# Kernel optimization log

Measured on AMD Instinct MI355X. Metric: run time of the kernel, lower is better.

Reference implementation:

```python
import jax, jax.numpy as jnp
import numpy as np

D = 2048
H = 16
HD = D // H
EPS = 1e-5

def setup_inputs() -> dict:
    key = jax.random.key(0)
    ks = jax.random.split(key, 7)
    B, S = 4, 2048
    scale = 1.0 / np.sqrt(D)
    return {
        "hidden_states": jax.random.normal(ks[0], (B, S, D), dtype=jnp.float32),
        "ln_gamma": jnp.ones((D,), dtype=jnp.float32),
        "ln_beta": jnp.zeros((D,), dtype=jnp.float32),
        "W_qkv": jax.random.normal(ks[1], (D, 3 * D), dtype=jnp.float32) * scale,
        "b_qkv": jnp.zeros((3 * D,), dtype=jnp.float32),
        "W_proj": jax.random.normal(ks[2], (D, D), dtype=jnp.float32) * scale,
        "b_proj": jnp.zeros((D,), dtype=jnp.float32),
    }

def reference(hidden_states, ln_gamma, ln_beta, W_qkv, b_qkv, W_proj, b_proj):
    B, S, _ = hidden_states.shape
    # LayerNorm (fused into QKV projection in the original kernel)
    mu = jnp.mean(hidden_states, axis=-1, keepdims=True)
    var = jnp.mean(jnp.square(hidden_states - mu), axis=-1, keepdims=True)
    x = (hidden_states - mu) * jax.lax.rsqrt(var + EPS) * ln_gamma + ln_beta
    # QKV projection
    qkv = jnp.einsum("bsd,de->bse", x, W_qkv) + b_qkv  # [B,S,3D]
    q, k, v = jnp.split(qkv, 3, axis=-1)
    # split heads -> [B,H,S,hd]
    q = q.reshape(B, S, H, HD).transpose(0, 2, 1, 3)
    k = k.reshape(B, S, H, HD).transpose(0, 2, 1, 3)
    v = v.reshape(B, S, H, HD).transpose(0, 2, 1, 3)
    # scaled causal attention
    scores = jnp.einsum("bhqd,bhkd->bhqk", q, k) / jnp.asarray(np.sqrt(HD), q.dtype)
    causal = jnp.tril(jnp.ones((S, S), dtype=bool))
    neg = jnp.finfo(scores.dtype).min
    scores = jnp.where(causal, scores, neg)
    attn = jax.nn.softmax(scores, axis=-1)
    out = jnp.einsum("bhqk,bhkd->bhqd", attn, v)
    # merge heads, output projection (dropout is identity in eval / p=0)
    out = out.transpose(0, 2, 1, 3).reshape(B, S, D)
    return jnp.einsum("bsd,de->bse", out, W_proj) + b_proj
```

## Files before the change

### kernel.cpp

```cpp
#include <hip/hip_runtime.h>
#include <cstdint>

typedef __attribute__((ext_vector_type(8))) short bf16x8;
typedef __attribute__((ext_vector_type(4))) float f32x4;
typedef unsigned short u16;
typedef unsigned int u32;

constexpr int D   = 2048;
constexpr int H   = 16;
constexpr int HD  = 128;
constexpr int BATCH = 4;
constexpr int S   = 2048;
constexpr int ROWS = BATCH * S;
constexpr int N3D = 3 * D;
constexpr int QKW = 2 * D;

__device__ __forceinline__ u16 f2bf(float f) {
    union { float f; u32 u; } v; v.f = f;
    u32 r = v.u + 0x7FFFu + ((v.u >> 16) & 1u);
    return (u16)(r >> 16);
}

__device__ __forceinline__ void gld_lds16(const u16* g, u16* l) {
    __builtin_amdgcn_global_load_lds(
        (const __attribute__((address_space(1))) void*)g,
        (__attribute__((address_space(3))) void*)l, 16, 0, 0);
}

__global__ __launch_bounds__(256) void ln_bf16_kernel(
    const float* __restrict__ x, const float* __restrict__ gamma,
    const float* __restrict__ beta, u16* __restrict__ out)
{
    const int row = blockIdx.x;
    const int t = threadIdx.x;
    const float* xr = x + (size_t)row * D;
    float4 a = ((const float4*)xr)[2*t];
    float4 b = ((const float4*)xr)[2*t+1];
    float s  = a.x+a.y+a.z+a.w + b.x+b.y+b.z+b.w;
    float ss = a.x*a.x+a.y*a.y+a.z*a.z+a.w*a.w + b.x*b.x+b.y*b.y+b.z*b.z+b.w*b.w;
    #pragma unroll
    for (int off = 32; off > 0; off >>= 1) {
        s  += __shfl_down(s, off);
        ss += __shfl_down(ss, off);
    }
    __shared__ float red[8];
    const int wave = t >> 6, lane = t & 63;
    if (lane == 0) { red[wave] = s; red[4+wave] = ss; }
    __syncthreads();
    const float mu   = (red[0]+red[1]+red[2]+red[3]) * (1.0f/D);
    const float var  = (red[4]+red[5]+red[6]+red[7]) * (1.0f/D) - mu*mu;
    const float rstd = rsqrtf(var + 1e-5f);
    float4 g0  = ((const float4*)gamma)[2*t];
    float4 g1  = ((const float4*)gamma)[2*t+1];
    float4 be0 = ((const float4*)beta)[2*t];
    float4 be1 = ((const float4*)beta)[2*t+1];
    union { uint4 v; u16 e[8]; } o;
    o.e[0] = f2bf((a.x-mu)*rstd*g0.x + be0.x);
    o.e[1] = f2bf((a.y-mu)*rstd*g0.y + be0.y);
    o.e[2] = f2bf((a.z-mu)*rstd*g0.z + be0.z);
    o.e[3] = f2bf((a.w-mu)*rstd*g0.w + be0.w);
    o.e[4] = f2bf((b.x-mu)*rstd*g1.x + be1.x);
    o.e[5] = f2bf((b.y-mu)*rstd*g1.y + be1.y);
    o.e[6] = f2bf((b.z-mu)*rstd*g1.z + be1.z);
    o.e[7] = f2bf((b.w-mu)*rstd*g1.w + be1.w);
    ((uint4*)(out + (size_t)row*D))[t] = o.v;
}

__global__ __launch_bounds__(256) void transpose_bf16_kernel(
    const float* __restrict__ in, u16* __restrict__ out, int K, int N)
{
    __shared__ u16 tile[64][65];
    const int tn0 = blockIdx.x * 64;
    const int tk0 = blockIdx.y * 64;
    const int t = threadIdx.x;
    const int tx = t & 63;
    const int ty = t >> 6;
    #pragma unroll
    for (int i = 0; i < 16; i++) {
        int k = ty + i*4;
        tile[k][tx] = f2bf(in[(size_t)(tk0+k)*N + tn0 + tx]);
    }
    __syncthreads();
    #pragma unroll
    for (int i = 0; i < 16; i++) {
        int n = ty + i*4;
        out[(size_t)(tn0+n)*K + tk0 + tx] = tile[tx][n];
    }
}

constexpr int BM = 256, BN = 256, BK = 32;

template<int MODE>
__global__ __launch_bounds__(512, 2) void gemm256_kernel(
    const u16* __restrict__ A, const u16* __restrict__ Bt,
    const float* __restrict__ bias, void* __restrict__ Cout,
    u16* __restrict__ vtb, int M, int N, int K)
{
    __shared__ u16 sA[4 * 8192];
    __shared__ u16 sB[4 * 8192];

    const int t = threadIdx.x;
    const int wave = t >> 6, lane = t & 63;
    const int lr = lane & 15, lq = lane >> 4;
    const int wm = wave >> 2, wn = wave & 3;
    const int m0 = blockIdx.y * BM, n0 = blockIdx.x * BN;

    const int g0 = t, g1 = t + 512;
    const int cs0 = ((g0 & 3) ^ ((g0 >> 3) & 3)) * 8;
    const int cs1 = ((g1 & 3) ^ ((g1 >> 3) & 3)) * 8;
    const u16* gA0 = A  + (size_t)(m0 + (g0 >> 2)) * K + cs0;
    const u16* gA1 = A  + (size_t)(m0 + (g1 >> 2)) * K + cs1;
    const u16* gB0 = Bt + (size_t)(n0 + (g0 >> 2)) * K + cs0;
    const u16* gB1 = Bt + (size_t)(n0 + (g1 >> 2)) * K + cs1;

    f32x4 acc[8][4];
    #pragma unroll
    for (int i = 0; i < 8; i++)
        #pragma unroll
        for (int j = 0; j < 4; j++)
            acc[i][j] = (f32x4)(0.0f);

    const int NT = K / BK;

    auto STAGE_A = [&](int slot, int kt) {
        u16* a = sA + slot * 8192 + wave * 512;
        gld_lds16(gA0 + kt * BK, a);
        gld_lds16(gA1 + kt * BK, a + 4096);
    };
    auto STAGE_B = [&](int slot, int kt) {
        u16* b = sB + slot * 8192 + wave * 512;
        gld_lds16(gB0 + kt * BK, b);
        gld_lds16(gB1 + kt * BK, b + 4096);
    };

    STAGE_A(0, 0); STAGE_B(0, 0);
    STAGE_A(1, 1); STAGE_B(1, 1);
    STAGE_A(2, 2); STAGE_B(2, 2);
    asm volatile("s_waitcnt vmcnt(8)" ::: "memory");
    __builtin_amdgcn_s_barrier();

    const int rblk = (lq ^ ((lr >> 1) & 3)) * 8;

    for (int kt = 0; kt < NT; ++kt) {
        const int tp = (kt + 3 < NT) ? (kt + 3) : (NT - 1);
        const int slot3 = (kt + 3) & 3;
        const u16* tAp = sA + (kt & 3) * 8192 + (wm * 128) * BK + rblk;
        const u16* tBp = sB + (kt & 3) * 8192 + (wn * 64)  * BK + rblk;

        bf16x8 bfr[4], af[4];
        #pragma unroll
        for (int nt = 0; nt < 4; nt++)
            bfr[nt] = *(const bf16x8*)(tBp + (nt * 16 + lr) * BK);
        #pragma unroll
        for (int mt = 0; mt < 4; mt++)
            af[mt] = *(const bf16x8*)(tAp + (mt * 16 + lr) * BK);
        STAGE_A(slot3, tp);
        __builtin_amdgcn_sched_barrier(0);
        __builtin_amdgcn_s_barrier();
        asm volatile("s_waitcnt lgkmcnt(0)" ::: "memory");
        __builtin_amdgcn_sched_barrier(0);
        __builtin_amdgcn_s_setprio(1);
        #pragma unroll
        for (int mt = 0; mt < 4; mt++)
            #pragma unroll
            for (int nt = 0; nt < 4; nt++)
                acc[mt][nt] = __builtin_amdgcn_mfma_f32_16x16x32_bf16(
                    af[mt], bfr[nt], acc[mt][nt], 0, 0, 0);
        __builtin_amdgcn_s_setprio(0);
        __builtin_amdgcn_sched_barrier(0);
        __builtin_amdgcn_s_barrier();

        #pragma unroll
        for (int mt = 0; mt < 4; mt++)
            af[mt] = *(const bf16x8*)(tAp + (64 + mt * 16 + lr) * BK);
        STAGE_B(slot3, tp);
        asm volatile("s_waitcnt vmcnt(8)" ::: "memory");
        __builtin_amdgcn_sched_barrier(0);
        __builtin_amdgcn_s_barrier();
        asm volatile("s_waitcnt lgkmcnt(0)" ::: "memory");
        __builtin_amdgcn_sched_barrier(0);
        __builtin_amdgcn_s_setprio(1);
        #pragma unroll
        for (int mt = 0; mt < 4; mt++)
            #pragma unroll
            for (int nt = 0; nt < 4; nt++)
                acc[4 + mt][nt] = __builtin_amdgcn_mfma_f32_16x16x32_bf16(
                    af[mt], bfr[nt], acc[4 + mt][nt], 0, 0, 0);
        __builtin_amdgcn_s_setprio(0);
        __builtin_amdgcn_sched_barrier(0);
        __builtin_amdgcn_s_barrier();
    }
    asm volatile("s_waitcnt vmcnt(0)" ::: "memory");

    #pragma unroll
    for (int i = 0; i < 8; i++) {
        const int row0 = m0 + wm * 128 + (i >> 2) * 64 + (i & 3) * 16 + lq * 4;
        #pragma unroll
        for (int nt = 0; nt < 4; nt++) {
            const int col = n0 + wn * 64 + nt * 16 + lr;
            const float bv = bias[col];
            float v[4];
            #pragma unroll
            for (int r = 0; r < 4; r++) v[r] = acc[i][nt][r] + bv;
            if (MODE == 0) {
                #pragma unroll
                for (int r = 0; r < 4; r++)
                    ((float*)Cout)[(size_t)(row0 + r) * N + col] = v[r];
            } else {
                if (n0 < QKW) {
                    #pragma unroll
                    for (int r = 0; r < 4; r++)
                        ((u16*)Cout)[(size_t)(row0 + r) * QKW + col] = f2bf(v[r]);
                } else {
                    const int vcol = col - QKW;
                    const int b = row0 >> 11, s0 = row0 & 2047;
                    ushort4 pk;
                    pk.x = f2bf(v[0]); pk.y = f2bf(v[1]);
                    pk.z = f2bf(v[2]); pk.w = f2bf(v[3]);
                    *(ushort4*)(vtb + ((size_t)(b*H + (vcol >> 7)) * HD
                                       + (vcol & 127)) * S + s0) = pk;
                }
            }
        }
    }
}

constexpr int TQ = 64, TK = 64;
constexpr int KPAD = 136;
constexpr int VPAD = 72;
constexpr int PPAD = 72;

__global__ __launch_bounds__(256) void attn_kernel(
    const u16* __restrict__ qkb, const u16* __restrict__ vtb,
    u16* __restrict__ ctx)
{
    __shared__ u16 sK[TK * KPAD];
    __shared__ u16 sVT[HD * VPAD];
    __shared__ u16 sP[4 * 16 * PPAD];

    const int flat = blockIdx.x;
    const int qt = 31 - (flat >> 6);
    const int bh = flat & 63;
    const int b  = bh >> 4, h = bh & 15;
    const int q0 = qt * TQ;
    const int t = threadIdx.x;
    const int wave = t >> 6, lane = t & 63;
    const int lr = lane & 15, lq = lane >> 4;

    const u16* baseQK = qkb + (size_t)b * S * QKW + h * HD;
    const u16* baseVT = vtb + (size_t)bh * HD * S;

    const int qrow = q0 + wave * 16 + lr;
    bf16x8 qf[4];
    #pragma unroll
    for (int kc = 0; kc < 4; kc++)
        qf[kc] = *(const bf16x8*)(baseQK + (size_t)qrow * QKW + kc*32 + lq*8);

    float m_r[4], l_r[4];
    f32x4 o[8];
    #pragma unroll
    for (int r = 0; r < 4; r++) { m_r[r] = -1e30f; l_r[r] = 0.0f; }
    #pragma unroll
    for (int j = 0; j < 8; j++) o[j] = (f32x4)(0.0f);

    const float scale = 0.08838834764831845f;
    const int nkt = qt + 1;

    for (int kt = 0; kt < nkt; kt++) {
        __syncthreads();
        #pragma unroll
        for (int i = 0; i < 4; i++) {
            int c = t + i * 256;
            int krow = c >> 4, kcol = (c & 15) * 8;
            uint4 v = *(const uint4*)(baseQK + D + (size_t)(kt*TK + krow) * QKW + kcol);
            *(uint4*)(sK + krow * KPAD + kcol) = v;
        }
        #pragma unroll
        for (int i = 0; i < 4; i++) {
            int c = t + i * 256;
            int vrow = c >> 3, coff = (c & 7) * 8;
            uint4 v = *(const uint4*)(baseVT + (size_t)vrow * S + kt*TK + coff);
            *(uint4*)(sVT + vrow * VPAD + coff) = v;
        }
        __syncthreads();

        f32x4 sc[4];
        #pragma unroll
        for (int nt = 0; nt < 4; nt++) sc[nt] = (f32x4)(0.0f);
        #pragma unroll
        for (int nt = 0; nt < 4; nt++)
            #pragma unroll
            for (int kc = 0; kc < 4; kc++) {
                bf16x8 kf = *(const bf16x8*)(sK + (nt*16 + lr) * KPAD + kc*32 + lq*8);
                sc[nt] = __builtin_amdgcn_mfma_f32_16x16x32_bf16(qf[kc], kf, sc[nt], 0, 0, 0);
            }

        const bool diag = (kt == qt);
        float rowmax[4] = {-1e30f, -1e30f, -1e30f, -1e30f};
        const int qgb = q0 + wave*16 + lq*4;
        #pragma unroll
        for (int nt = 0; nt < 4; nt++)
            #pragma unroll
            for (int r = 0; r < 4; r++) {
                float sv = sc[nt][r] * scale;
                if (diag) {
                    const int kg = kt*TK + nt*16 + lr;
                    if (kg > qgb + r) sv = -1e30f;
                }
                sc[nt][r] = sv;
                rowmax[r] = fmaxf(rowmax[r], sv);
            }
        #pragma unroll
        for (int mask = 1; mask < 16; mask <<= 1)
            #pragma unroll
            for (int r = 0; r < 4; r++)
                rowmax[r] = fmaxf(rowmax[r], __shfl_xor(rowmax[r], mask));

        float alpha[4];
        #pragma unroll
        for (int r = 0; r < 4; r++) {
            float nm = fmaxf(m_r[r], rowmax[r]);
            alpha[r] = __expf(m_r[r] - nm);
            m_r[r] = nm;
        }

        u16* pw = sP + wave * 16 * PPAD;
        #pragma unroll
        for (int nt = 0; nt < 4; nt++) {
            #pragma unroll
            for (int r = 0; r < 4; r++) {
                float p = __expf(sc[nt][r] - m_r[r]);
                sc[nt][r] = p;
                pw[(lq*4 + r) * PPAD + nt*16 + lr] = f2bf(p);
            }
        }
        #pragma unroll
        for (int r = 0; r < 4; r++) {
            float psum = sc[0][r] + sc[1][r] + sc[2][r] + sc[3][r];
            l_r[r] = l_r[r] * alpha[r] + psum;
        }
        #pragma unroll
        for (int j = 0; j < 8; j++)
            #pragma unroll
            for (int r = 0; r < 4; r++)
                o[j][r] *= alpha[r];

        #pragma unroll
        for (int kc2 = 0; kc2 < 2; kc2++) {
            bf16x8 pa = *(const bf16x8*)(pw + lr * PPAD + kc2*32 + lq*8);
            #pragma unroll
            for (int n2 = 0; n2 < 8; n2++) {
                bf16x8 vb = *(const bf16x8*)(sVT + (n2*16 + lr) * VPAD + kc2*32 + lq*8);
                o[n2] = __builtin_amdgcn_mfma_f32_16x16x32_bf16(pa, vb, o[n2], 0, 0, 0);
            }
        }
    }

    #pragma unroll
    for (int mask = 1; mask < 16; mask <<= 1)
        #pragma unroll
        for (int r = 0; r < 4; r++)
            l_r[r] += __shfl_xor(l_r[r], mask);
    float inv_l[4];
    #pragma unroll
    for (int r = 0; r < 4; r++) inv_l[r] = 1.0f / l_r[r];
    #pragma unroll
    for (int n2 = 0; n2 < 8; n2++)
        #pragma unroll
        for (int r = 0; r < 4; r++) {
            const int qg = q0 + wave*16 + lq*4 + r;
            const float v = o[n2][r] * inv_l[r];
            ctx[(size_t)(b * S + qg) * D + h * HD + n2*16 + lr] = f2bf(v);
        }
}

extern "C" void kernel_launch(void* const* d_in, const int* in_sizes, int n_in,
                              void* d_out, int out_size, void* d_ws, size_t ws_size,
                              hipStream_t stream) {
    const float* hs    = (const float*)d_in[0];
    const float* gamma = (const float*)d_in[1];
    const float* beta  = (const float*)d_in[2];
    const float* Wqkv  = (const float*)d_in[3];
    const float* bqkv  = (const float*)d_in[4];
    const float* Wproj = (const float*)d_in[5];
    const float* bproj = (const float*)d_in[6];

    char* ws = (char*)d_ws;
    size_t off = 0;
    u16* xb   = (u16*)(ws + off); off += (size_t)ROWS * D * 2;
    u16* wtq  = (u16*)(ws + off); off += (size_t)N3D * D * 2;
    u16* wtp  = (u16*)(ws + off); off += (size_t)D * D * 2;
    u16* qkb  = (u16*)(ws + off); off += (size_t)ROWS * QKW * 2;
    u16* vtb  = (u16*)(ws + off); off += (size_t)ROWS * D * 2;
    u16* ctxb = (u16*)(ws + off);

    ln_bf16_kernel<<<ROWS, 256, 0, stream>>>(hs, gamma, beta, xb);
    transpose_bf16_kernel<<<dim3(N3D/64, D/64), 256, 0, stream>>>(Wqkv, wtq, D, N3D);
    transpose_bf16_kernel<<<dim3(D/64,   D/64), 256, 0, stream>>>(Wproj, wtp, D, D);
    gemm256_kernel<2><<<dim3(N3D/BN, ROWS/BM), 512, 0, stream>>>(
        xb, wtq, bqkv, qkb, vtb, ROWS, N3D, D);
    attn_kernel<<<dim3((S/TQ) * BATCH * H), 256, 0, stream>>>(qkb, vtb, ctxb);
    gemm256_kernel<0><<<dim3(D/BN, ROWS/BM), 512, 0, stream>>>(
        ctxb, wtp, bproj, (float*)d_out, nullptr, ROWS, D, D);
}
```

Measured before the change: 610.3 us.

## Double-buffer attention K/V tiles with async LDS loads and swizzled layout

The attention kernel now stages K and V^T tiles directly into LDS with global_load_lds, using two buffers so the next tile is fetched while the current one is computed. This removes the register round-trip and one barrier per iteration. The padded LDS rows are replaced by XOR-swizzled unpadded rows to avoid bank conflicts, and s_setprio raises wave priority around the MFMA loops. The change relies on the async loads being complete before the single remaining barrier, and it doubles LDS use for K and V, which may lower occupancy.

```diff
diff --git a/kernel.cpp b/kernel.cpp
--- a/kernel.cpp
+++ b/kernel.cpp
@@ -226,16 +226,14 @@
 }
 
 constexpr int TQ = 64, TK = 64;
-constexpr int KPAD = 136;
-constexpr int VPAD = 72;
 constexpr int PPAD = 72;
 
 __global__ __launch_bounds__(256) void attn_kernel(
     const u16* __restrict__ qkb, const u16* __restrict__ vtb,
     u16* __restrict__ ctx)
 {
-    __shared__ u16 sK[TK * KPAD];
-    __shared__ u16 sVT[HD * VPAD];
+    __shared__ u16 sK[2 * TK * HD];
+    __shared__ u16 sVT[2 * HD * TK];
     __shared__ u16 sP[4 * 16 * PPAD];
 
     const int flat = blockIdx.x;
@@ -256,6 +254,36 @@
     for (int kc = 0; kc < 4; kc++)
         qf[kc] = *(const bf16x8*)(baseQK + (size_t)qrow * QKW + kc*32 + lq*8);
 
+    const u16* kptr0; const u16* kptr1; const u16* kptr2; const u16* kptr3;
+    {
+        const int r0 = wave*16 + (lane>>4);
+        kptr0 = baseQK + D + (size_t)(r0     ) * QKW + (((lane&15) ^ ( 0 + (lane>>4))) * 8);
+        kptr1 = baseQK + D + (size_t)(r0 +  4) * QKW + (((lane&15) ^ ( 4 + (lane>>4))) * 8);
+        kptr2 = baseQK + D + (size_t)(r0 +  8) * QKW + (((lane&15) ^ ( 8 + (lane>>4))) * 8);
+        kptr3 = baseQK + D + (size_t)(r0 + 12) * QKW + (((lane&15) ^ (12 + (lane>>4))) * 8);
+    }
+    const int vcbs = ((lane & 7) ^ (lane >> 3)) * 8;
+    const int vr0 = wave*32 + (lane>>3);
+    const u16* vptr0 = baseVT + (size_t)(vr0     ) * S + vcbs;
+    const u16* vptr1 = baseVT + (size_t)(vr0 +  8) * S + vcbs;
+    const u16* vptr2 = baseVT + (size_t)(vr0 + 16) * S + vcbs;
+    const u16* vptr3 = baseVT + (size_t)(vr0 + 24) * S + vcbs;
+
+    auto STAGE = [&](int buf, int kt) {
+        u16* kd = sK  + buf * 8192 + wave * 2048;
+        u16* vd = sVT + buf * 8192 + wave * 2048;
+        const size_t ko = (size_t)(kt * TK) * QKW;
+        const int vo = kt * TK;
+        gld_lds16(kptr0 + ko, kd);
+        gld_lds16(kptr1 + ko, kd + 512);
+        gld_lds16(kptr2 + ko, kd + 1024);
+        gld_lds16(kptr3 + ko, kd + 1536);
+        gld_lds16(vptr0 + vo, vd);
+        gld_lds16(vptr1 + vo, vd + 512);
+        gld_lds16(vptr2 + vo, vd + 1024);
+        gld_lds16(vptr3 + vo, vd + 1536);
+    };
+
     float m_r[4], l_r[4];
     f32x4 o[8];
     #pragma unroll
@@ -266,34 +294,28 @@
     const float scale = 0.08838834764831845f;
     const int nkt = qt + 1;
 
+    STAGE(0, 0);
+
     for (int kt = 0; kt < nkt; kt++) {
         __syncthreads();
-        #pragma unroll
-        for (int i = 0; i < 4; i++) {
-            int c = t + i * 256;
-            int krow = c >> 4, kcol = (c & 15) * 8;
-            uint4 v = *(const uint4*)(baseQK + D + (size_t)(kt*TK + krow) * QKW + kcol);
-            *(uint4*)(sK + krow * KPAD + kcol) = v;
-        }
-        #pragma unroll
-        for (int i = 0; i < 4; i++) {
-            int c = t + i * 256;
-            int vrow = c >> 3, coff = (c & 7) * 8;
-            uint4 v = *(const uint4*)(baseVT + (size_t)vrow * S + kt*TK + coff);
-            *(uint4*)(sVT + vrow * VPAD + coff) = v;
-        }
-        __syncthreads();
+        if (kt + 1 < nkt) STAGE((kt + 1) & 1, kt + 1);
+
+        const u16* Kb = sK  + (kt & 1) * 8192;
+        const u16* Vb = sVT + (kt & 1) * 8192;
 
         f32x4 sc[4];
         #pragma unroll
         for (int nt = 0; nt < 4; nt++) sc[nt] = (f32x4)(0.0f);
+        __builtin_amdgcn_s_setprio(1);
         #pragma unroll
         for (int nt = 0; nt < 4; nt++)
             #pragma unroll
             for (int kc = 0; kc < 4; kc++) {
-                bf16x8 kf = *(const bf16x8*)(sK + (nt*16 + lr) * KPAD + kc*32 + lq*8);
+                bf16x8 kf = *(const bf16x8*)(Kb + (nt*16 + lr) * HD
+                                             + (((kc*4 + lq) ^ lr) * 8));
                 sc[nt] = __builtin_amdgcn_mfma_f32_16x16x32_bf16(qf[kc], kf, sc[nt], 0, 0, 0);
             }
+        __builtin_amdgcn_s_setprio(0);
 
         const bool diag = (kt == qt);
         float rowmax[4] = {-1e30f, -1e30f, -1e30f, -1e30f};
@@ -348,11 +370,14 @@
         #pragma unroll
         for (int kc2 = 0; kc2 < 2; kc2++) {
             bf16x8 pa = *(const bf16x8*)(pw + lr * PPAD + kc2*32 + lq*8);
+            __builtin_amdgcn_s_setprio(1);
             #pragma unroll
             for (int n2 = 0; n2 < 8; n2++) {
-                bf16x8 vb = *(const bf16x8*)(sVT + (n2*16 + lr) * VPAD + kc2*32 + lq*8);
+                bf16x8 vb = *(const bf16x8*)(Vb + (n2*16 + lr) * TK
+                                             + ((((kc2*4) + lq) ^ (lr & 7)) * 8));
                 o[n2] = __builtin_amdgcn_mfma_f32_16x16x32_bf16(pa, vb, o[n2], 0, 0, 0);
             }
+            __builtin_amdgcn_s_setprio(0);
         }
     }
 
```

Result: faster. 577.8 us (-5.3%).
